# Performance work log

Measured on AMD Instinct MI355X. Metric: run time of the kernel, lower is better.

Reference implementation:

```python
import jax, jax.numpy as jnp
import numpy as np

B, V_IN, V_OUT, C_IN, C_OUT, K, NNZ = 16, 1024, 4096, 128, 256, 18, 16384

def setup_inputs() -> dict:
    key = jax.random.key(0)
    ks = jax.random.split(key, 10)
    def lin(k, fan_in, fan_out):
        s = 1.0 / np.sqrt(fan_in)
        return jax.random.normal(k, (fan_in, fan_out), jnp.float32) * s
    return {
        "x": jax.random.normal(ks[0], (B, V_IN, C_IN), jnp.float32),
        "vals": jax.random.uniform(ks[1], (NNZ,), jnp.float32),
        "W1": lin(ks[2], 1 * C_IN, C_OUT),
        "b1": jnp.zeros((C_OUT,), jnp.float32),
        "Wd3": lin(ks[3], (K // 3) * C_IN, C_OUT // 4),
        "bd3": jnp.zeros((C_OUT // 4,), jnp.float32),
        "W2d3": lin(ks[4], (K // 3 * 2) * C_IN, C_OUT // 4),
        "b2d3": jnp.zeros((C_OUT // 4,), jnp.float32),
        "Wf": lin(ks[5], K * C_IN, C_OUT // 2),
        "bf": jnp.zeros((C_OUT // 2,), jnp.float32),
        "rows": jax.random.randint(ks[6], (NNZ,), 0, V_OUT, jnp.int32),
        "cols": jax.random.randint(ks[7], (NNZ,), 0, V_IN, jnp.int32),
        "spiral_idx": jax.random.randint(ks[8], (V_OUT, K), 0, V_OUT, jnp.int32),
    }

def _pool(x, rows, cols, vals, dim_size):
    # sparse upsample: gather cols, scale, scatter-add to rows
    gathered = x[:, cols, :] * vals[None, :, None]  # [B, nnz, C]
    return jnp.zeros((x.shape[0], dim_size, x.shape[2]), x.dtype).at[:, rows, :].add(gathered)

def _spiral_conv(feat, idx, W, b):
    # gather fixed spiral neighborhoods then shared linear layer
    Bz, V, C = feat.shape[0], idx.shape[0], feat.shape[2]
    g = feat[:, idx.reshape(-1), :].reshape(Bz, V, idx.shape[1] * C)  # [B, V, K*C]
    return g @ W + b

def reference(x, vals, W1, b1, Wd3, bd3, W2d3, b2d3, Wf, bf, rows, cols, spiral_idx):
    out = _pool(x, rows, cols, vals, V_OUT)  # [B, V_OUT, C_IN]
    k = spiral_idx.shape[1]
    short_cut = _spiral_conv(out, spiral_idx[:, :1], W1, b1)
    p_d3 = _spiral_conv(out, spiral_idx[:, : k // 3], Wd3, bd3)
    p_2d3 = _spiral_conv(out, spiral_idx[:, : k // 3 * 2], W2d3, b2d3)
    p = _spiral_conv(out, spiral_idx, Wf, bf)
    f = jnp.concatenate((p, p_2d3, p_d3), axis=2)  # [B, V_OUT, C_OUT]
    return jax.nn.relu(short_cut + f)
```

## Files before the change

### kernel.cpp

```cpp
#include <hip/hip_runtime.h>
#include <hip/hip_bf16.h>

#define B_SZ   16
#define V_IN   1024
#define V_OUT  4096
#define C_IN   128
#define C_OUT  256
#define K_NB   18
#define NNZ    16384
#define K_GEMM (K_NB * C_IN)
#define BK     64
#define NKT    (K_GEMM / BK)

typedef __attribute__((ext_vector_type(8))) short bf16x8;
typedef __attribute__((ext_vector_type(4))) float f32x4;

#define GLOAD16(src, dst) __builtin_amdgcn_global_load_lds( \
    (const __attribute__((address_space(1))) unsigned int*)(src), \
    (__attribute__((address_space(3))) unsigned int*)(dst), 16, 0, 0)

#define MFMA16(a_, b_, c_) __builtin_amdgcn_mfma_f32_16x16x32_bf16((a_), (b_), (c_), 0, 0, 0)

__global__ __launch_bounds__(1024) void csr_kernel(const int* __restrict__ rows,
                                                   int* __restrict__ offsets,
                                                   int* __restrict__ perm) {
    __shared__ int cnt[V_OUT];
    __shared__ int wsum[16];
    const int t = threadIdx.x;
    const int lane = t & 63, wid = t >> 6;
#pragma unroll
    for (int i = t; i < V_OUT; i += 1024) cnt[i] = 0;
    __syncthreads();
#pragma unroll
    for (int n = t; n < NNZ; n += 1024) atomicAdd(&cnt[rows[n]], 1);
    __syncthreads();
    const int base4 = t * 4;
    int c0 = cnt[base4], c1 = cnt[base4 + 1], c2 = cnt[base4 + 2], c3 = cnt[base4 + 3];
    int tot = c0 + c1 + c2 + c3;
    int v = tot;
#pragma unroll
    for (int d = 1; d < 64; d <<= 1) {
        int u = __shfl_up(v, d);
        if (lane >= d) v += u;
    }
    if (lane == 63) wsum[wid] = v;
    __syncthreads();
    int wbase = 0;
#pragma unroll
    for (int w = 0; w < 16; ++w) wbase += (w < wid) ? wsum[w] : 0;
    int incl = wbase + v;
    int excl = incl - tot;
    offsets[base4]     = excl;
    offsets[base4 + 1] = excl + c0;
    offsets[base4 + 2] = excl + c0 + c1;
    offsets[base4 + 3] = excl + c0 + c1 + c2;
    if (t == 1023) offsets[V_OUT] = incl;
    __syncthreads();
    cnt[base4]     = excl;
    cnt[base4 + 1] = excl + c0;
    cnt[base4 + 2] = excl + c0 + c1;
    cnt[base4 + 3] = excl + c0 + c1 + c2;
    __syncthreads();
#pragma unroll
    for (int n = t; n < NNZ; n += 1024) {
        int pos = atomicAdd(&cnt[rows[n]], 1);
        perm[pos] = n;
    }
}

__global__ __launch_bounds__(512) void pool_kernel(
    const float* __restrict__ x, const float* __restrict__ vals,
    const int* __restrict__ cols, const int* __restrict__ offsets,
    const int* __restrict__ perm, __hip_bfloat16* __restrict__ pool) {
    int r = blockIdx.x;
    int t = threadIdx.x;
    int b = t >> 5, c4 = t & 31;
    int j0 = offsets[r], j1 = offsets[r + 1];
    const float4* xb = (const float4*)x + (size_t)b * (V_IN * 32);
    float4 acc = {0.f, 0.f, 0.f, 0.f};
    for (int j = j0; j < j1; ++j) {
        int n = perm[j];
        float v = vals[n];
        float4 xv = xb[cols[n] * 32 + c4];
        acc.x += v * xv.x; acc.y += v * xv.y; acc.z += v * xv.z; acc.w += v * xv.w;
    }
    ushort4 o;
    o.x = __builtin_bit_cast(unsigned short, __float2bfloat16(acc.x));
    o.y = __builtin_bit_cast(unsigned short, __float2bfloat16(acc.y));
    o.z = __builtin_bit_cast(unsigned short, __float2bfloat16(acc.z));
    o.w = __builtin_bit_cast(unsigned short, __float2bfloat16(acc.w));
    ((ushort4*)pool)[((size_t)b * V_OUT + r) * 32 + c4] = o;
}

__global__ __launch_bounds__(256) void wcomb_kernel(
    const float* __restrict__ W1, const float* __restrict__ Wd3,
    const float* __restrict__ W2d3, const float* __restrict__ Wf,
    const float* __restrict__ b1, const float* __restrict__ bd3,
    const float* __restrict__ b2d3, const float* __restrict__ bf,
    __hip_bfloat16* __restrict__ wTs, float* __restrict__ bias) {
    const int blk = blockIdx.x;
    const int t   = threadIdx.x;
    if (blk == NKT * 4) {
        float v = b1[t];
        if (t < 128)      v += bf[t];
        else if (t < 192) v += b2d3[t - 128];
        else              v += bd3[t - 192];
        bias[t] = v;
        return;
    }
    const int kt = blk >> 2, part = blk & 3;
    __shared__ __hip_bfloat16 img[4096];
    const int k0 = kt * 64;

    auto put = [&](int cl, int col7, int kl, float v) {
        int kb    = (kl >> 3) << 4;
        int kslot = kb ^ (col7 << 4);
        int idx   = (((cl << 3) | (kslot >> 4)) << 3) | (kl & 7);
        img[idx] = __float2bfloat16(v);
    };

    if (part < 2) {
        const int cbase = part << 6;
        for (int i = t; i < 4096; i += 256) {
            int kl = i >> 6, cl = i & 63;
            int col = cbase + cl, r = k0 + kl;
            float v = Wf[r * 128 + col];
            if (r < 128) v += W1[r * 256 + col];
            put(cl, col & 7, kl, v);
        }
    } else if (part == 2) {
        for (int i = t; i < 4096; i += 256) {
            int kl = i >> 6, cl = i & 63;
            int r = k0 + kl;
            float v = (r < 1536) ? W2d3[r * 64 + cl] : 0.f;
            if (r < 128) v += W1[r * 256 + 128 + cl];
            put(cl, cl & 7, kl, v);
        }
    } else {
        for (int i = t; i < 4096; i += 256) {
            int kl = i >> 6, cl = i & 63;
            int r = k0 + kl;
            float v = (r < 768) ? Wd3[r * 64 + cl] : 0.f;
            if (r < 128) v += W1[r * 256 + 192 + cl];
            put(cl, cl & 7, kl, v);
        }
    }
    __syncthreads();
    ulonglong2* dst = (ulonglong2*)(wTs + (size_t)kt * 16384 + part * 4096);
    const ulonglong2* srcv = (const ulonglong2*)img;
#pragma unroll
    for (int i = t; i < 512; i += 256) dst[i] = srcv[i];
}

__global__ __launch_bounds__(1024, 4) void gemm_kernel(
    const __hip_bfloat16* __restrict__ pool,
    const __hip_bfloat16* __restrict__ wTs,
    const float* __restrict__ bias,
    const int* __restrict__ spiral,
    float* __restrict__ out)
{
    __shared__ __align__(16) char smem[149504];
    int* spl = (int*)(smem + 131072);

    const int tid  = threadIdx.x;
    const int lane = tid & 63;
    const int wid  = tid >> 6;
    const int wc   = wid & 3;
    const int wm   = (wid >> 2) << 6;

    const int bid = blockIdx.x;
    const int bm  = ((bid & 7) << 5) + (bid >> 3);
    const int b   = bm >> 4;
    const int v0  = (bm & 15) << 8;

    for (int i = tid; i < 256 * K_NB; i += 1024) {
        int j = i >> 8, row = i & 255;
        spl[i] = spiral[(v0 + row) * K_NB + j];
    }
    asm volatile("s_waitcnt vmcnt(0) lgkmcnt(0)" ::: "memory");
    __builtin_amdgcn_s_barrier();

    const char* poolBytes = (const char*)(pool + (size_t)b * V_OUT * C_IN);
    const char* wTsBytes  = (const char*)wTs;
    const int sb = ((tid & 7) << 4) ^ (((tid >> 3) & 7) << 4);

    auto stageA = [&](int kt) {
        const int j   = kt >> 1;
        const int c0b = (kt & 1) << 7;
        char* dst = smem + ((kt & 1) << 15);
#pragma unroll
        for (int ch = 0; ch < 2; ++ch) {
            int flat = (ch << 10) + tid;
            int sidx = spl[(j << 8) + (flat >> 3)];
            GLOAD16(poolBytes + ((size_t)sidx << 8) + (c0b + sb), dst + flat * 16);
        }
    };
    auto stageB = [&](int kt) {
        const char* src = wTsBytes + ((size_t)kt << 15);
        char* dst = smem + 65536 + ((kt & 1) << 15);
#pragma unroll
        for (int ch = 0; ch < 2; ++ch) {
            int off = ((ch << 10) + tid) << 4;
            GLOAD16(src + off, dst + off);
        }
    };

    const int l15   = lane & 15;
    const int swm   = (lane & 7) << 4;
    const int klane = (lane >> 4) << 4;
    const int aBase = (wm + l15) << 7;
    const int bOff0 = (((2 * wc)     << 4) + l15) << 7;
    const int bOff1 = (((2 * wc + 1) << 4) + l15) << 7;
    const int bOff2 = (((8 + wc)     << 4) + l15) << 7;
    const int bOff3 = (((12 + wc)    << 4) + l15) << 7;

    f32x4 acc[4][4] = {};

    stageA(0);
    stageB(0);

    for (int kt = 0; kt < NKT; ++kt) {
        const int s = kt & 1;
        const char* As = smem + (s << 15);
        const char* Bs = smem + 65536 + (s << 15);

        if (kt + 1 < NKT) {
            stageA(kt + 1);
            stageB(kt + 1);
            asm volatile("s_waitcnt vmcnt(4)" ::: "memory");
        } else {
            asm volatile("s_waitcnt vmcnt(0)" ::: "memory");
        }
        __builtin_amdgcn_s_barrier();
        __builtin_amdgcn_sched_barrier(0);

        const bool doMid   = kt < 24;
        const bool doShort = kt < 12;

#pragma unroll
        for (int ks = 0; ks < 2; ++ks) {
            const int kk = (ks * 64 + klane) ^ swm;
            bf16x8 a0 = *(const bf16x8*)(As + aBase + (0 << 11) + kk);
            bf16x8 a1 = *(const bf16x8*)(As + aBase + (1 << 11) + kk);
            bf16x8 a2 = *(const bf16x8*)(As + aBase + (2 << 11) + kk);
            bf16x8 a3 = *(const bf16x8*)(As + aBase + (3 << 11) + kk);
            bf16x8 bb0 = *(const bf16x8*)(Bs + bOff0 + kk);
            bf16x8 bb1 = *(const bf16x8*)(Bs + bOff1 + kk);
            __builtin_amdgcn_s_setprio(1);
            acc[0][0] = MFMA16(a0, bb0, acc[0][0]);
            acc[1][0] = MFMA16(a1, bb0, acc[1][0]);
            acc[2][0] = MFMA16(a2, bb0, acc[2][0]);
            acc[3][0] = MFMA16(a3, bb0, acc[3][0]);
            acc[0][1] = MFMA16(a0, bb1, acc[0][1]);
            acc[1][1] = MFMA16(a1, bb1, acc[1][1]);
            acc[2][1] = MFMA16(a2, bb1, acc[2][1]);
            acc[3][1] = MFMA16(a3, bb1, acc[3][1]);
            __builtin_amdgcn_s_setprio(0);
            if (doMid) {
                bf16x8 bb2 = *(const bf16x8*)(Bs + bOff2 + kk);
                __builtin_amdgcn_s_setprio(1);
                acc[0][2] = MFMA16(a0, bb2, acc[0][2]);
                acc[1][2] = MFMA16(a1, bb2, acc[1][2]);
                acc[2][2] = MFMA16(a2, bb2, acc[2][2]);
                acc[3][2] = MFMA16(a3, bb2, acc[3][2]);
                __builtin_amdgcn_s_setprio(0);
            }
            if (doShort) {
                bf16x8 bb3 = *(const bf16x8*)(Bs + bOff3 + kk);
                __builtin_amdgcn_s_setprio(1);
                acc[0][3] = MFMA16(a0, bb3, acc[0][3]);
                acc[1][3] = MFMA16(a1, bb3, acc[1][3]);
                acc[2][3] = MFMA16(a2, bb3, acc[2][3]);
                acc[3][3] = MFMA16(a3, bb3, acc[3][3]);
                __builtin_amdgcn_s_setprio(0);
            }
        }

        __builtin_amdgcn_s_barrier();
        __builtin_amdgcn_sched_barrier(0);
    }

    const int nt[4] = {2 * wc, 2 * wc + 1, 8 + wc, 12 + wc};
#pragma unroll
    for (int ni = 0; ni < 4; ++ni) {
        int col = (nt[ni] << 4) + l15;
        float bz = bias[col];
#pragma unroll
        for (int mi = 0; mi < 4; ++mi) {
            int row0 = v0 + wm + mi * 16 + ((lane >> 4) << 2);
#pragma unroll
            for (int r4 = 0; r4 < 4; ++r4) {
                float v = acc[mi][ni][r4] + bz;
                out[((size_t)(b * V_OUT + row0 + r4)) * C_OUT + col] = v > 0.f ? v : 0.f;
            }
        }
    }
}

extern "C" void kernel_launch(void* const* d_in, const int* in_sizes, int n_in,
                              void* d_out, int out_size, void* d_ws, size_t ws_size,
                              hipStream_t stream) {
    const float* x     = (const float*)d_in[0];
    const float* vals  = (const float*)d_in[1];
    const float* W1    = (const float*)d_in[2];
    const float* b1    = (const float*)d_in[3];
    const float* Wd3   = (const float*)d_in[4];
    const float* bd3   = (const float*)d_in[5];
    const float* W2d3  = (const float*)d_in[6];
    const float* b2d3  = (const float*)d_in[7];
    const float* Wf    = (const float*)d_in[8];
    const float* bf    = (const float*)d_in[9];
    const int*   rows  = (const int*)d_in[10];
    const int*   cols  = (const int*)d_in[11];
    const int*   spiral= (const int*)d_in[12];
    float* out = (float*)d_out;

    char* ws = (char*)d_ws;
    __hip_bfloat16* pool = (__hip_bfloat16*)ws;
    __hip_bfloat16* wTs  = (__hip_bfloat16*)(ws + 16777216);
    float* bias          = (float*)(ws + 16777216 + 1179648);
    int*   offsets       = (int*)(ws + 16777216 + 1179648 + 1024);
    int*   perm          = offsets + V_OUT + 4;

    csr_kernel<<<1, 1024, 0, stream>>>(rows, offsets, perm);
    pool_kernel<<<V_OUT, 512, 0, stream>>>(x, vals, cols, offsets, perm, pool);
    wcomb_kernel<<<NKT * 4 + 1, 256, 0, stream>>>(W1, Wd3, W2d3, Wf, b1, bd3, b2d3, bf, wTs, bias);
    gemm_kernel<<<256, 1024, 0, stream>>>(pool, wTs, bias, spiral, out);
}
```

Before: 114.9 us.

## Pack col/val pairs in CSR, coalesce spiral load, defer B staging mid-loop

The CSR build now writes packed (col, val) pairs in sorted order, so the pool kernel reads one float2 per nonzero instead of chasing perm into two separate arrays. The GEMM now copies the spiral index tile contiguously into shared memory, changing it to row-major layout, and stageA indexes it accordingly. The B-tile prefetch for the next k-step moves from before the barrier to after the first k-substep's MFMAs, and the wait count drops to vmcnt(2). This spreads weight loads across compute, at the cost of possible shared-memory bank conflicts on spl reads and a B load that lands later relative to its use.

```diff
diff --git a/kernel.cpp b/kernel.cpp
--- a/kernel.cpp
+++ b/kernel.cpp
@@ -22,8 +22,10 @@
 #define MFMA16(a_, b_, c_) __builtin_amdgcn_mfma_f32_16x16x32_bf16((a_), (b_), (c_), 0, 0, 0)
 
 __global__ __launch_bounds__(1024) void csr_kernel(const int* __restrict__ rows,
+                                                   const int* __restrict__ cols,
+                                                   const float* __restrict__ vals,
                                                    int* __restrict__ offsets,
-                                                   int* __restrict__ perm) {
+                                                   float2* __restrict__ pcv) {
     __shared__ int cnt[V_OUT];
     __shared__ int wsum[16];
     const int t = threadIdx.x;
@@ -64,14 +66,13 @@
 #pragma unroll
     for (int n = t; n < NNZ; n += 1024) {
         int pos = atomicAdd(&cnt[rows[n]], 1);
-        perm[pos] = n;
+        pcv[pos] = make_float2(__int_as_float(cols[n]), vals[n]);
     }
 }
 
 __global__ __launch_bounds__(512) void pool_kernel(
-    const float* __restrict__ x, const float* __restrict__ vals,
-    const int* __restrict__ cols, const int* __restrict__ offsets,
-    const int* __restrict__ perm, __hip_bfloat16* __restrict__ pool) {
+    const float* __restrict__ x, const int* __restrict__ offsets,
+    const float2* __restrict__ pcv, __hip_bfloat16* __restrict__ pool) {
     int r = blockIdx.x;
     int t = threadIdx.x;
     int b = t >> 5, c4 = t & 31;
@@ -79,9 +80,10 @@
     const float4* xb = (const float4*)x + (size_t)b * (V_IN * 32);
     float4 acc = {0.f, 0.f, 0.f, 0.f};
     for (int j = j0; j < j1; ++j) {
-        int n = perm[j];
-        float v = vals[n];
-        float4 xv = xb[cols[n] * 32 + c4];
+        float2 cv = pcv[j];
+        int col = __float_as_int(cv.x);
+        float v = cv.y;
+        float4 xv = xb[col * 32 + c4];
         acc.x += v * xv.x; acc.y += v * xv.y; acc.z += v * xv.z; acc.w += v * xv.w;
     }
     ushort4 o;
@@ -173,10 +175,7 @@
     const int b   = bm >> 4;
     const int v0  = (bm & 15) << 8;
 
-    for (int i = tid; i < 256 * K_NB; i += 1024) {
-        int j = i >> 8, row = i & 255;
-        spl[i] = spiral[(v0 + row) * K_NB + j];
-    }
+    for (int i = tid; i < 256 * K_NB; i += 1024) spl[i] = spiral[v0 * K_NB + i];
     asm volatile("s_waitcnt vmcnt(0) lgkmcnt(0)" ::: "memory");
     __builtin_amdgcn_s_barrier();
 
@@ -191,7 +190,7 @@
 #pragma unroll
         for (int ch = 0; ch < 2; ++ch) {
             int flat = (ch << 10) + tid;
-            int sidx = spl[(j << 8) + (flat >> 3)];
+            int sidx = spl[(flat >> 3) * K_NB + j];
             GLOAD16(poolBytes + ((size_t)sidx << 8) + (c0b + sb), dst + flat * 16);
         }
     };
@@ -226,8 +225,7 @@
 
         if (kt + 1 < NKT) {
             stageA(kt + 1);
-            stageB(kt + 1);
-            asm volatile("s_waitcnt vmcnt(4)" ::: "memory");
+            asm volatile("s_waitcnt vmcnt(2)" ::: "memory");
         } else {
             asm volatile("s_waitcnt vmcnt(0)" ::: "memory");
         }
@@ -274,6 +272,7 @@
                 acc[3][3] = MFMA16(a3, bb3, acc[3][3]);
                 __builtin_amdgcn_s_setprio(0);
             }
+            if (ks == 0 && kt + 1 < NKT) stageB(kt + 1);
         }
 
         __builtin_amdgcn_s_barrier();
@@ -320,10 +319,10 @@
     __hip_bfloat16* wTs  = (__hip_bfloat16*)(ws + 16777216);
     float* bias          = (float*)(ws + 16777216 + 1179648);
     int*   offsets       = (int*)(ws + 16777216 + 1179648 + 1024);
-    int*   perm          = offsets + V_OUT + 4;
-
-    csr_kernel<<<1, 1024, 0, stream>>>(rows, offsets, perm);
-    pool_kernel<<<V_OUT, 512, 0, stream>>>(x, vals, cols, offsets, perm, pool);
+    float2* pcv          = (float2*)(ws + 16777216 + 1179648 + 1024 + 16640);
+
+    csr_kernel<<<1, 1024, 0, stream>>>(rows, cols, vals, offsets, pcv);
+    pool_kernel<<<V_OUT, 512, 0, stream>>>(x, offsets, pcv, pool);
     wcomb_kernel<<<NKT * 4 + 1, 256, 0, stream>>>(W1, Wd3, W2d3, Wf, b1, bd3, b2d3, bf, wTs, bias);
     gemm_kernel<<<256, 1024, 0, stream>>>(pool, wTs, bias, spiral, out);
 }
```

New measurement: 115.2 us. No clear change (+0.2%).
